# Optimization experiments

Measured on AMD Instinct MI355X. Metric: run time of the kernel, lower is better.

The kernel has to match this reference:

```python
import jax, jax.numpy as jnp
import numpy as np

IN_DIM, HID, B, T = 128, 512, 32, 2048
TAU_X, TAU = 200.0, 5


def setup_inputs() -> dict:
    key = jax.random.key(0)
    ks = jax.random.split(key, 12)
    s = 0.05
    return {
        "in_seq": jax.random.normal(ks[0], (B, T, IN_DIM), jnp.float32),
        "We1": jax.random.normal(ks[1], (IN_DIM, HID), jnp.float32) * s,
        "be1": jnp.zeros((HID,), jnp.float32),
        "We2": jax.random.normal(ks[2], (HID, HID), jnp.float32) * s,
        "be2": jnp.zeros((HID,), jnp.float32),
        "We3": jax.random.normal(ks[3], (HID, HID), jnp.float32) * s,
        "be3": jnp.zeros((HID,), jnp.float32),
        # decoder: Linear+tanh, Linear+tanh
        "Wd1": jax.random.normal(ks[4], (HID, HID), jnp.float32) * s,
        "bd1": jnp.zeros((HID,), jnp.float32),
        "Wd2": jax.random.normal(ks[5], (HID, IN_DIM), jnp.float32) * s,
        "bd2": jnp.zeros((IN_DIM,), jnp.float32),
        # recurrent weight (torch: randn * 0.1)
        "W": jax.random.normal(ks[6], (HID, HID), jnp.float32) * 0.1,
    }


def reference(in_seq, We1, be1, We2, be2, We3, be3, Wd1, bd1, Wd2, bd2, W):
    def encoder(u):
        h = jnp.tanh(u @ We1 + be1)
        h = jnp.tanh(h @ We2 + be2)
        return jnp.tanh(h @ We3 + be3)

    def decoder(h):
        h = jnp.tanh(h @ Wd1 + bd1)
        return jnp.tanh(h @ Wd2 + bd2)

    x_seq = encoder(in_seq)  # [B, T, H]
    Tlen = in_seq.shape[1]
    # teacher forcing flag per step: t % tau == 0 and t > 0
    t_idx = jnp.arange(Tlen)
    tf_flags = (t_idx % TAU == 0) & (t_idx > 0)

    xs_T = jnp.swapaxes(x_seq, 0, 1)  # [T, B, H]

    def step(x, inp):
        flag, xs_t = inp
        x = jnp.where(flag, xs_t, x)
        dx = -x + jnp.tanh(x) @ W.T
        x = x + dx / TAU_X
        return x, decoder(x)  # per-step prediction [B, in_dim]

    x0 = x_seq[:, 0, :]
    _, preds = jax.lax.scan(step, x0, (tf_flags, xs_T))  # preds: [T, B, in_dim]
    x_pred = jnp.swapaxes(preds, 0, 1)  # [B, T, in_dim]
    x_recon = decoder(x_seq)  # [B, T, in_dim]
    return (x_pred, x_recon)
```

## Files before the change

### kernel.cpp

```cpp
#include <hip/hip_runtime.h>
#include <stdint.h>

#define B_SZ  32
#define T_SZ  2048
#define IN_D  128
#define HID   512
#define NCHAIN 410
#define INV_TAUX 0.005f

typedef __attribute__((ext_vector_type(8))) short bf16x8;
typedef __attribute__((ext_vector_type(4))) float f32x4;
typedef __attribute__((ext_vector_type(4))) float float4v;
typedef __attribute__((ext_vector_type(4))) unsigned short u16x4;
typedef __attribute__((ext_vector_type(8))) unsigned short u16x8;

#define MFMA(b, a, c) __builtin_amdgcn_mfma_f32_16x16x32_bf16((b), (a), (c), 0, 0, 0)

__device__ __forceinline__ unsigned short f2bf(float x) {
  union { float f; unsigned int u; } v; v.f = x;
  unsigned int r = v.u + 0x7FFFu + ((v.u >> 16) & 1u);
  return (unsigned short)(r >> 16);
}
__device__ __forceinline__ float bf2f(unsigned short b) {
  union { unsigned int u; float f; } v; v.u = ((unsigned int)b) << 16;
  return v.f;
}
__device__ __forceinline__ float fast_tanh(float x) {
  float ax = fabsf(x);
  float e = __expf(-2.0f * ax);
  float r = (1.0f - e) * __builtin_amdgcn_rcpf(1.0f + e);
  return x < 0.0f ? -r : r;
}
__device__ __forceinline__ void gload_lds16(const void* g, void* l) {
  __builtin_amdgcn_global_load_lds(
      reinterpret_cast<__attribute__((address_space(1))) void*>(reinterpret_cast<uintptr_t>(g)),
      reinterpret_cast<__attribute__((address_space(3))) void*>(reinterpret_cast<uintptr_t>(l)),
      16, 0, 0);
}


__global__ __launch_bounds__(512) void enc5_k(
    const float* __restrict__ in_seq,
    const unsigned short* __restrict__ wt,
    const float* __restrict__ be1, const float* __restrict__ be2,
    const float* __restrict__ be3,
    const unsigned short* __restrict__ Wd1t,
    const unsigned short* __restrict__ Wd2t,
    const float* __restrict__ bd1, const float* __restrict__ bd2,
    unsigned short* __restrict__ xseq,
    float* __restrict__ outr)
{
  __shared__ __attribute__((aligned(16))) unsigned short sH[64 * 512];
  unsigned short* sA = sH;

  const int tid = threadIdx.x;
  const int m0 = blockIdx.x * 64;
  const int wave = tid >> 6, lane = tid & 63;
  const int wn = wave;
  const int lrow = lane & 15, lhi = lane >> 4, sw = lrow & 7;

#pragma unroll
  for (int p = 0; p < 2; ++p) {
    int id = (p << 9) + tid;
    int row = id >> 4, cc = id & 15;
    const float* src = in_seq + (size_t)(m0 + row) * IN_D + (cc << 3);
    float4v u0 = *(const float4v*)src;
    float4v u1 = *(const float4v*)(src + 4);
    u16x8 h;
    h[0] = f2bf(u0[0]); h[1] = f2bf(u0[1]); h[2] = f2bf(u0[2]); h[3] = f2bf(u0[3]);
    h[4] = f2bf(u1[0]); h[5] = f2bf(u1[1]); h[6] = f2bf(u1[2]); h[7] = f2bf(u1[3]);
    int slot = (cc & 8) | ((cc & 7) ^ (row & 7));
    *(u16x8*)(sA + (row << 7) + (slot << 3)) = h;
  }
  __syncthreads();

  f32x4 acc[4][4];
  const unsigned short* Bts[3] = {wt, wt + 65536, wt + 327680};
  const float* bss[3] = {be1, be2, be3};

  for (int l = 0; l < 3; ++l) {
    const int lstr = (l == 0) ? 128 : 512;
    const int nk = (l == 0) ? 4 : 16;
    const unsigned short* bl = Bts[l] + (lane << 3);
    const int nfb = (wn << 2) * nk;
    const float* bias = bss[l];

#pragma unroll
    for (int m = 0; m < 4; ++m)
#pragma unroll
      for (int n = 0; n < 4; ++n) acc[m][n] = (f32x4){0.f, 0.f, 0.f, 0.f};

    bf16x8 b0[4], b1[4];
#pragma unroll
    for (int n = 0; n < 4; ++n)
      b0[n] = *(const bf16x8*)(bl + ((nfb + n * nk) << 9));

    for (int kk = 0; kk < nk; kk += 2) {
#pragma unroll
      for (int n = 0; n < 4; ++n)
        b1[n] = *(const bf16x8*)(bl + ((nfb + n * nk + kk + 1) << 9));
      {
        const int c = (kk << 2) + lhi;
        const int slot = (c & ~7) | ((c & 7) ^ sw);
        bf16x8 af[4];
#pragma unroll
        for (int m = 0; m < 4; ++m)
          af[m] = *(const bf16x8*)(sH + (m * 16 + lrow) * lstr + (slot << 3));
#pragma unroll
        for (int n = 0; n < 4; ++n)
#pragma unroll
          for (int m = 0; m < 4; ++m)
            acc[m][n] = MFMA(b0[n], af[m], acc[m][n]);
      }
      if (kk + 2 < nk) {
#pragma unroll
        for (int n = 0; n < 4; ++n)
          b0[n] = *(const bf16x8*)(bl + ((nfb + n * nk + kk + 2) << 9));
      }
      {
        const int c = ((kk + 1) << 2) + lhi;
        const int slot = (c & ~7) | ((c & 7) ^ sw);
        bf16x8 af[4];
#pragma unroll
        for (int m = 0; m < 4; ++m)
          af[m] = *(const bf16x8*)(sH + (m * 16 + lrow) * lstr + (slot << 3));
#pragma unroll
        for (int n = 0; n < 4; ++n)
#pragma unroll
          for (int m = 0; m < 4; ++m)
            acc[m][n] = MFMA(b1[n], af[m], acc[m][n]);
      }
    }
    __syncthreads();
#pragma unroll
    for (int n = 0; n < 4; ++n) {
      const int col0 = (wn << 6) + n * 16 + (lhi << 2);
      const float4v bv = *(const float4v*)(bias + col0);
      const int c2 = col0 >> 3;
#pragma unroll
      for (int m = 0; m < 4; ++m) {
        const int row = m * 16 + lrow;
        const int slot2 = (c2 & ~7) | ((c2 & 7) ^ (row & 7));
        u16x4 h;
#pragma unroll
        for (int q = 0; q < 4; ++q) h[q] = f2bf(fast_tanh(acc[m][n][q] + bv[q]));
        *(u16x4*)(sH + (row << 9) + (slot2 << 3) + (col0 & 7)) = h;
      }
    }
    __syncthreads();
  }

#pragma unroll
  for (int p = 0; p < 8; ++p) {
    int id = (p << 9) + tid;
    int row = id >> 6, cc = id & 63;
    int slot = (cc & ~7) | ((cc & 7) ^ (row & 7));
    u16x8 v = *(const u16x8*)(sH + (row << 9) + (slot << 3));
    *(u16x8*)(xseq + ((size_t)(m0 + row) << 9) + (cc << 3)) = v;
  }

#pragma unroll
  for (int m = 0; m < 4; ++m)
#pragma unroll
    for (int n = 0; n < 4; ++n) acc[m][n] = (f32x4){0.f, 0.f, 0.f, 0.f};

  {
    const unsigned short* bl = Wd1t + (lane << 3);
    const int nfb = (wn << 2) << 4;
    bf16x8 b0[4], b1[4];
#pragma unroll
    for (int n = 0; n < 4; ++n)
      b0[n] = *(const bf16x8*)(bl + ((nfb + (n << 4)) << 9));
    for (int kk = 0; kk < 16; kk += 2) {
#pragma unroll
      for (int n = 0; n < 4; ++n)
        b1[n] = *(const bf16x8*)(bl + ((nfb + (n << 4) + kk + 1) << 9));
      {
        const int c = (kk << 2) + lhi;
        const int slot = (c & ~7) | ((c & 7) ^ sw);
        bf16x8 af[4];
#pragma unroll
        for (int m = 0; m < 4; ++m)
          af[m] = *(const bf16x8*)(sH + ((m * 16 + lrow) << 9) + (slot << 3));
#pragma unroll
        for (int n = 0; n < 4; ++n)
#pragma unroll
          for (int m = 0; m < 4; ++m)
            acc[m][n] = MFMA(b0[n], af[m], acc[m][n]);
      }
      if (kk + 2 < 16) {
#pragma unroll
        for (int n = 0; n < 4; ++n)
          b0[n] = *(const bf16x8*)(bl + ((nfb + (n << 4) + kk + 2) << 9));
      }
      {
        const int c = ((kk + 1) << 2) + lhi;
        const int slot = (c & ~7) | ((c & 7) ^ sw);
        bf16x8 af[4];
#pragma unroll
        for (int m = 0; m < 4; ++m)
          af[m] = *(const bf16x8*)(sH + ((m * 16 + lrow) << 9) + (slot << 3));
#pragma unroll
        for (int n = 0; n < 4; ++n)
#pragma unroll
          for (int m = 0; m < 4; ++m)
            acc[m][n] = MFMA(b1[n], af[m], acc[m][n]);
      }
    }
  }
  __syncthreads();
#pragma unroll
  for (int n = 0; n < 4; ++n) {
    const int col0 = (wn << 6) + n * 16 + (lhi << 2);
    const float4v bv = *(const float4v*)(bd1 + col0);
    const int c2 = col0 >> 3;
#pragma unroll
    for (int m = 0; m < 4; ++m) {
      const int row = m * 16 + lrow;
      const int slot2 = (c2 & ~7) | ((c2 & 7) ^ (row & 7));
      u16x4 h;
#pragma unroll
      for (int q = 0; q < 4; ++q) h[q] = f2bf(fast_tanh(acc[m][n][q] + bv[q]));
      *(u16x4*)(sH + (row << 9) + (slot2 << 3) + (col0 & 7)) = h;
    }
  }
  __syncthreads();

  f32x4 acc2[4];
#pragma unroll
  for (int m = 0; m < 4; ++m) acc2[m] = (f32x4){0.f, 0.f, 0.f, 0.f};

  {
    const unsigned short* bl = Wd2t + (lane << 3);
    const int nfb = wn << 4;
    bf16x8 c0, c1;
    c0 = *(const bf16x8*)(bl + ((nfb + 0) << 9));
    for (int kk = 0; kk < 16; kk += 2) {
      c1 = *(const bf16x8*)(bl + ((nfb + kk + 1) << 9));
      {
        const int c = (kk << 2) + lhi;
        const int slot = (c & ~7) | ((c & 7) ^ sw);
#pragma unroll
        for (int m = 0; m < 4; ++m) {
          bf16x8 af = *(const bf16x8*)(sH + ((m * 16 + lrow) << 9) + (slot << 3));
          acc2[m] = MFMA(c0, af, acc2[m]);
        }
      }
      if (kk + 2 < 16)
        c0 = *(const bf16x8*)(bl + ((nfb + kk + 2) << 9));
      {
        const int c = ((kk + 1) << 2) + lhi;
        const int slot = (c & ~7) | ((c & 7) ^ sw);
#pragma unroll
        for (int m = 0; m < 4; ++m) {
          bf16x8 af = *(const bf16x8*)(sH + ((m * 16 + lrow) << 9) + (slot << 3));
          acc2[m] = MFMA(c1, af, acc2[m]);
        }
      }
    }
  }
  {
    const int col0 = (wn << 4) + (lhi << 2);
    const float4v bv = *(const float4v*)(bd2 + col0);
#pragma unroll
    for (int m = 0; m < 4; ++m) {
      const int row = m * 16 + lrow;
      float4v o;
#pragma unroll
      for (int q = 0; q < 4; ++q) o[q] = fast_tanh(acc2[m][q] + bv[q]);
      *(float4v*)(outr + (size_t)(m0 + row) * IN_D + col0) = o;
    }
  }
}

__global__ __launch_bounds__(512) void dec_fused_k(
    const unsigned short* __restrict__ X,
    const unsigned short* __restrict__ Wd1t,
    const unsigned short* __restrict__ Wd2t,
    const float* __restrict__ bd1, const float* __restrict__ bd2,
    float* __restrict__ out)
{
  __shared__ __attribute__((aligned(16))) unsigned short sH[64 * 512];
  unsigned short* sX = sH;

  const int tid = threadIdx.x;
  const int m0 = blockIdx.x * 64;
  const int wave = tid >> 6, lane = tid & 63;
  const int wn = wave;
  const int lrow = lane & 15, lhi = lane >> 4, sw = lrow & 7;

  char* lX = (char*)sX + tid * 16;
#pragma unroll
  for (int p = 0; p < 8; ++p) {
    int id = (p << 9) + tid;
    int row = id >> 6, cc = id & 63;
    int gcc = (cc & ~7) | ((cc & 7) ^ (row & 7));
    gload_lds16(X + ((size_t)(m0 + row) << 9) + (gcc << 3), lX + (p << 13));
  }
  __syncthreads();

  f32x4 acc[4][4];
#pragma unroll
  for (int m = 0; m < 4; ++m)
#pragma unroll
    for (int n = 0; n < 4; ++n) acc[m][n] = (f32x4){0.f, 0.f, 0.f, 0.f};

  {
    const unsigned short* bl = Wd1t + (lane << 3);
    const int nfb = (wn << 2) << 4;
    bf16x8 b0[4], b1[4];
#pragma unroll
    for (int n = 0; n < 4; ++n)
      b0[n] = *(const bf16x8*)(bl + ((nfb + (n << 4)) << 9));
    for (int kk = 0; kk < 16; kk += 2) {
#pragma unroll
      for (int n = 0; n < 4; ++n)
        b1[n] = *(const bf16x8*)(bl + ((nfb + (n << 4) + kk + 1) << 9));
      {
        const int c = (kk << 2) + lhi;
        const int slot = (c & ~7) | ((c & 7) ^ sw);
        bf16x8 af[4];
#pragma unroll
        for (int m = 0; m < 4; ++m)
          af[m] = *(const bf16x8*)(sX + ((m * 16 + lrow) << 9) + (slot << 3));
#pragma unroll
        for (int n = 0; n < 4; ++n)
#pragma unroll
          for (int m = 0; m < 4; ++m)
            acc[m][n] = MFMA(b0[n], af[m], acc[m][n]);
      }
      if (kk + 2 < 16) {
#pragma unroll
        for (int n = 0; n < 4; ++n)
          b0[n] = *(const bf16x8*)(bl + ((nfb + (n << 4) + kk + 2) << 9));
      }
      {
        const int c = ((kk + 1) << 2) + lhi;
        const int slot = (c & ~7) | ((c & 7) ^ sw);
        bf16x8 af[4];
#pragma unroll
        for (int m = 0; m < 4; ++m)
          af[m] = *(const bf16x8*)(sX + ((m * 16 + lrow) << 9) + (slot << 3));
#pragma unroll
        for (int n = 0; n < 4; ++n)
#pragma unroll
          for (int m = 0; m < 4; ++m)
            acc[m][n] = MFMA(b1[n], af[m], acc[m][n]);
      }
    }
  }
  __syncthreads();
#pragma unroll
  for (int n = 0; n < 4; ++n) {
    const int col0 = (wn << 6) + n * 16 + (lhi << 2);
    const float4v bv = *(const float4v*)(bd1 + col0);
    const int c2 = col0 >> 3;
#pragma unroll
    for (int m = 0; m < 4; ++m) {
      const int row = m * 16 + lrow;
      const int slot2 = (c2 & ~7) | ((c2 & 7) ^ (row & 7));
      u16x4 h;
#pragma unroll
      for (int q = 0; q < 4; ++q) h[q] = f2bf(fast_tanh(acc[m][n][q] + bv[q]));
      *(u16x4*)(sH + (row << 9) + (slot2 << 3) + (col0 & 7)) = h;
    }
  }
  __syncthreads();

  f32x4 acc2[4];
#pragma unroll
  for (int m = 0; m < 4; ++m) acc2[m] = (f32x4){0.f, 0.f, 0.f, 0.f};

  {
    const unsigned short* bl = Wd2t + (lane << 3);
    const int nfb = wn << 4;
    bf16x8 c0, c1;
    c0 = *(const bf16x8*)(bl + ((nfb + 0) << 9));
    for (int kk = 0; kk < 16; kk += 2) {
      c1 = *(const bf16x8*)(bl + ((nfb + kk + 1) << 9));
      {
        const int c = (kk << 2) + lhi;
        const int slot = (c & ~7) | ((c & 7) ^ sw);
#pragma unroll
        for (int m = 0; m < 4; ++m) {
          bf16x8 af = *(const bf16x8*)(sH + ((m * 16 + lrow) << 9) + (slot << 3));
          acc2[m] = MFMA(c0, af, acc2[m]);
        }
      }
      if (kk + 2 < 16)
        c0 = *(const bf16x8*)(bl + ((nfb + kk + 2) << 9));
      {
        const int c = ((kk + 1) << 2) + lhi;
        const int slot = (c & ~7) | ((c & 7) ^ sw);
#pragma unroll
        for (int m = 0; m < 4; ++m) {
          bf16x8 af = *(const bf16x8*)(sH + ((m * 16 + lrow) << 9) + (slot << 3));
          acc2[m] = MFMA(c1, af, acc2[m]);
        }
      }
    }
  }
  {
    const int col0 = (wn << 4) + (lhi << 2);
    const float4v bv = *(const float4v*)(bd2 + col0);
#pragma unroll
    for (int m = 0; m < 4; ++m) {
      const int row = m * 16 + lrow;
      float4v o;
#pragma unroll
      for (int q = 0; q < 4; ++q) o[q] = fast_tanh(acc2[m][q] + bv[q]);
      *(float4v*)(out + (size_t)(m0 + row) * IN_D + col0) = o;
    }
  }
}

__global__ __launch_bounds__(512) void rec_all_k(
    const unsigned short* __restrict__ Wrec,
    unsigned short* __restrict__ xsall)
{
  __shared__ float xst[32][516];
  __shared__ __attribute__((aligned(16))) unsigned short sA[32 * 512];

  const int tid = threadIdx.x;
  const int chain = blockIdx.x;
  const int t0 = chain * 5;
  const int wave = tid >> 6, lane = tid & 63;
  const int wn = wave;
  const int lrow = lane & 15, lhi = lane >> 4, sw = lrow & 7;

#pragma unroll
  for (int p = 0; p < 4; ++p) {
    int id = (p << 9) + tid;
    int row = id >> 6, c8 = (id & 63) << 3;
    u16x8 v = *(const u16x8*)(xsall + (((size_t)row * T_SZ + t0) << 9) + c8);
#pragma unroll
    for (int e = 0; e < 8; ++e) xst[row][c8 + e] = bf2f(v[e]);
  }
  __syncthreads();

  const unsigned short* bl = Wrec + (lane << 3);
  const int nfb = (wn << 2) << 4;

  for (int s = 0; s < 5; ++s) {
#pragma unroll
    for (int p = 0; p < 4; ++p) {
      int id = (p << 9) + tid;
      int row = id >> 6, cc = id & 63;
      int gc = (cc & ~7) | ((cc & 7) ^ (row & 7));
      const float* src = &xst[row][gc << 3];
      float4v u0 = *(const float4v*)src;
      float4v u1 = *(const float4v*)(src + 4);
      u16x8 h;
      h[0] = f2bf(fast_tanh(u0[0])); h[1] = f2bf(fast_tanh(u0[1]));
      h[2] = f2bf(fast_tanh(u0[2])); h[3] = f2bf(fast_tanh(u0[3]));
      h[4] = f2bf(fast_tanh(u1[0])); h[5] = f2bf(fast_tanh(u1[1]));
      h[6] = f2bf(fast_tanh(u1[2])); h[7] = f2bf(fast_tanh(u1[3]));
      *(u16x8*)(sA + (row << 9) + (cc << 3)) = h;
    }
    __syncthreads();

    f32x4 acc[2][4];
#pragma unroll
    for (int m = 0; m < 2; ++m)
#pragma unroll
      for (int n = 0; n < 4; ++n) acc[m][n] = (f32x4){0.f, 0.f, 0.f, 0.f};

    bf16x8 b0[4], b1[4];
#pragma unroll
    for (int n = 0; n < 4; ++n)
      b0[n] = *(const bf16x8*)(bl + ((nfb + (n << 4)) << 9));
    for (int kk = 0; kk < 16; kk += 2) {
#pragma unroll
      for (int n = 0; n < 4; ++n)
        b1[n] = *(const bf16x8*)(bl + ((nfb + (n << 4) + kk + 1) << 9));
      {
        const int c = (kk << 2) + lhi;
        const int slot = (c & ~7) | ((c & 7) ^ sw);
        bf16x8 af0 = *(const bf16x8*)(sA + (lrow << 9) + (slot << 3));
        bf16x8 af1 = *(const bf16x8*)(sA + ((16 + lrow) << 9) + (slot << 3));
#pragma unroll
        for (int n = 0; n < 4; ++n) {
          acc[0][n] = MFMA(b0[n], af0, acc[0][n]);
          acc[1][n] = MFMA(b0[n], af1, acc[1][n]);
        }
      }
      if (kk + 2 < 16) {
#pragma unroll
        for (int n = 0; n < 4; ++n)
          b0[n] = *(const bf16x8*)(bl + ((nfb + (n << 4) + kk + 2) << 9));
      }
      {
        const int c = ((kk + 1) << 2) + lhi;
        const int slot = (c & ~7) | ((c & 7) ^ sw);
        bf16x8 af0 = *(const bf16x8*)(sA + (lrow << 9) + (slot << 3));
        bf16x8 af1 = *(const bf16x8*)(sA + ((16 + lrow) << 9) + (slot << 3));
#pragma unroll
        for (int n = 0; n < 4; ++n) {
          acc[0][n] = MFMA(b1[n], af0, acc[0][n]);
          acc[1][n] = MFMA(b1[n], af1, acc[1][n]);
        }
      }
    }
    __syncthreads();

    const int t = t0 + s;
#pragma unroll
    for (int n = 0; n < 4; ++n) {
      const int col0 = (wn << 6) + n * 16 + (lhi << 2);
#pragma unroll
      for (int m = 0; m < 2; ++m) {
        const int row = m * 16 + lrow;
        float4v x = *(const float4v*)(&xst[row][col0]);
        float4v xn;
#pragma unroll
        for (int q = 0; q < 4; ++q) xn[q] = x[q] + (acc[m][n][q] - x[q]) * INV_TAUX;
        *(float4v*)(&xst[row][col0]) = xn;
        if (t < T_SZ) {
          u16x4 h;
#pragma unroll
          for (int q = 0; q < 4; ++q) h[q] = f2bf(xn[q]);
          *(u16x4*)(xsall + ((size_t)row * T_SZ + t) * HID + col0) = h;
        }
      }
    }
    __syncthreads();
  }
}

__global__ void prep_k(const float* __restrict__ We1, const float* __restrict__ We2,
                       const float* __restrict__ We3, const float* __restrict__ Wd1,
                       const float* __restrict__ Wd2, const float* __restrict__ W,
                       unsigned short* __restrict__ wt) {
  int idx = blockIdx.x * blockDim.x + threadIdx.x;
  if (idx >= 1179648) return;
  unsigned short v;
  if (idx < 65536) {
    int i = idx, lane = (i >> 3) & 63, t2 = i >> 9;
    int kk = t2 & 3, nf = t2 >> 2;
    int n = (nf << 4) + (lane & 15), k = (kk << 5) + ((lane >> 4) << 3) + (i & 7);
    v = f2bf(We1[k * 512 + n]);
  } else if (idx < 327680) {
    int i = idx - 65536, lane = (i >> 3) & 63, t2 = i >> 9;
    int kk = t2 & 15, nf = t2 >> 4;
    int n = (nf << 4) + (lane & 15), k = (kk << 5) + ((lane >> 4) << 3) + (i & 7);
    v = f2bf(We2[k * 512 + n]);
  } else if (idx < 589824) {
    int i = idx - 327680, lane = (i >> 3) & 63, t2 = i >> 9;
    int kk = t2 & 15, nf = t2 >> 4;
    int n = (nf << 4) + (lane & 15), k = (kk << 5) + ((lane >> 4) << 3) + (i & 7);
    v = f2bf(We3[k * 512 + n]);
  } else if (idx < 851968) {
    int i = idx - 589824, lane = (i >> 3) & 63, t2 = i >> 9;
    int kk = t2 & 15, nf = t2 >> 4;
    int n = (nf << 4) + (lane & 15), k = (kk << 5) + ((lane >> 4) << 3) + (i & 7);
    v = f2bf(Wd1[k * 512 + n]);
  } else if (idx < 917504) {
    int i = idx - 851968, lane = (i >> 3) & 63, t2 = i >> 9;
    int kk = t2 & 15, nf = t2 >> 4;
    int n = (nf << 4) + (lane & 15), k = (kk << 5) + ((lane >> 4) << 3) + (i & 7);
    v = f2bf(Wd2[k * 128 + n]);
  } else {
    int i = idx - 917504, lane = (i >> 3) & 63, t2 = i >> 9;
    int kk = t2 & 15, nf = t2 >> 4;
    int n = (nf << 4) + (lane & 15), k = (kk << 5) + ((lane >> 4) << 3) + (i & 7);
    v = f2bf(W[(n << 9) + k]);
  }
  wt[idx] = v;
}

__global__ void sentinel_k(float* out, float v) { out[0] = v; }

extern "C" void kernel_launch(void* const* d_in, const int* in_sizes, int n_in,
                              void* d_out, int out_size, void* d_ws, size_t ws_size,
                              hipStream_t stream) {
  const float* in_seq = (const float*)d_in[0];
  const float* We1 = (const float*)d_in[1];
  const float* be1 = (const float*)d_in[2];
  const float* We2 = (const float*)d_in[3];
  const float* be2 = (const float*)d_in[4];
  const float* We3 = (const float*)d_in[5];
  const float* be3 = (const float*)d_in[6];
  const float* Wd1 = (const float*)d_in[7];
  const float* bd1 = (const float*)d_in[8];
  const float* Wd2 = (const float*)d_in[9];
  const float* bd2 = (const float*)d_in[10];
  const float* W   = (const float*)d_in[11];

  const int NROW = B_SZ * T_SZ;
  const size_t OFF_XSEQ = 0;
  const size_t OFF_WT   = (size_t)NROW * HID * 2;
  const size_t REQUIRED = OFF_WT + 2359296;

  float* outp = (float*)d_out;
  float* outr = outp + (size_t)NROW * IN_D;

  if (ws_size < REQUIRED) {
    sentinel_k<<<1, 1, 0, stream>>>(outp, (float)(ws_size >> 20));
    return;
  }

  char* ws = (char*)d_ws;
  unsigned short* xseq = (unsigned short*)(ws + OFF_XSEQ);
  unsigned short* wt   = (unsigned short*)(ws + OFF_WT);
  unsigned short* Wd1t = wt + 589824;
  unsigned short* Wd2t = wt + 851968;
  unsigned short* Wrec = wt + 917504;

  prep_k<<<4608, 256, 0, stream>>>(We1, We2, We3, Wd1, Wd2, W, wt);
  enc5_k<<<1024, 512, 0, stream>>>(in_seq, wt, be1, be2, be3,
                                   Wd1t, Wd2t, bd1, bd2, xseq, outr);
  rec_all_k<<<NCHAIN, 512, 0, stream>>>(Wrec, xseq);
  dec_fused_k<<<1024, 512, 0, stream>>>(xseq, Wd1t, Wd2t, bd1, bd2, outp);
}
```

Measured before the change: 439.7 us.

## Double decoder tile rows per block and stage recurrent output stores through LDS

The decoder kernel now handles 128 rows per block with 1024 threads (16 waves split 2x8), so each loaded weight fragment serves twice as many rows and the grid is halved. The recurrent kernel now writes its bf16 state into shared memory first and then stores it to global memory with 16-byte coalesced writes, replacing scattered 8-byte stores. This adds an extra barrier per recurrent step. The decoder's doubled LDS (128 KB) and 1024-thread blocks limit occupancy to one block per CU.

New measurement: 461.6 us. 1.05x slower.

```diff
diff --git a/kernel.cpp b/kernel.cpp
--- a/kernel.cpp
+++ b/kernel.cpp
@@ -273,29 +273,30 @@
   }
 }
 
-__global__ __launch_bounds__(512) void dec_fused_k(
+__global__ __launch_bounds__(1024) void dec_fused_k(
     const unsigned short* __restrict__ X,
     const unsigned short* __restrict__ Wd1t,
     const unsigned short* __restrict__ Wd2t,
     const float* __restrict__ bd1, const float* __restrict__ bd2,
     float* __restrict__ out)
 {
-  __shared__ __attribute__((aligned(16))) unsigned short sH[64 * 512];
+  __shared__ __attribute__((aligned(16))) unsigned short sH[128 * 512];
   unsigned short* sX = sH;
 
   const int tid = threadIdx.x;
-  const int m0 = blockIdx.x * 64;
+  const int m0 = blockIdx.x * 128;
   const int wave = tid >> 6, lane = tid & 63;
-  const int wn = wave;
+  const int wm = wave >> 3, wn = wave & 7;
+  const int rb = wm << 6;
   const int lrow = lane & 15, lhi = lane >> 4, sw = lrow & 7;
 
   char* lX = (char*)sX + tid * 16;
 #pragma unroll
   for (int p = 0; p < 8; ++p) {
-    int id = (p << 9) + tid;
+    int id = (p << 10) + tid;
     int row = id >> 6, cc = id & 63;
     int gcc = (cc & ~7) | ((cc & 7) ^ (row & 7));
-    gload_lds16(X + ((size_t)(m0 + row) << 9) + (gcc << 3), lX + (p << 13));
+    gload_lds16(X + ((size_t)(m0 + row) << 9) + (gcc << 3), lX + (p << 14));
   }
   __syncthreads();
 
@@ -322,7 +323,7 @@
         bf16x8 af[4];
 #pragma unroll
         for (int m = 0; m < 4; ++m)
-          af[m] = *(const bf16x8*)(sX + ((m * 16 + lrow) << 9) + (slot << 3));
+          af[m] = *(const bf16x8*)(sX + ((rb + m * 16 + lrow) << 9) + (slot << 3));
 #pragma unroll
         for (int n = 0; n < 4; ++n)
 #pragma unroll
@@ -340,7 +341,7 @@
         bf16x8 af[4];
 #pragma unroll
         for (int m = 0; m < 4; ++m)
-          af[m] = *(const bf16x8*)(sX + ((m * 16 + lrow) << 9) + (slot << 3));
+          af[m] = *(const bf16x8*)(sX + ((rb + m * 16 + lrow) << 9) + (slot << 3));
 #pragma unroll
         for (int n = 0; n < 4; ++n)
 #pragma unroll
@@ -357,7 +358,7 @@
     const int c2 = col0 >> 3;
 #pragma unroll
     for (int m = 0; m < 4; ++m) {
-      const int row = m * 16 + lrow;
+      const int row = rb + m * 16 + lrow;
       const int slot2 = (c2 & ~7) | ((c2 & 7) ^ (row & 7));
       u16x4 h;
 #pragma unroll
@@ -383,7 +384,7 @@
         const int slot = (c & ~7) | ((c & 7) ^ sw);
 #pragma unroll
         for (int m = 0; m < 4; ++m) {
-          bf16x8 af = *(const bf16x8*)(sH + ((m * 16 + lrow) << 9) + (slot << 3));
+          bf16x8 af = *(const bf16x8*)(sH + ((rb + m * 16 + lrow) << 9) + (slot << 3));
           acc2[m] = MFMA(c0, af, acc2[m]);
         }
       }
@@ -394,7 +395,7 @@
         const int slot = (c & ~7) | ((c & 7) ^ sw);
 #pragma unroll
         for (int m = 0; m < 4; ++m) {
-          bf16x8 af = *(const bf16x8*)(sH + ((m * 16 + lrow) << 9) + (slot << 3));
+          bf16x8 af = *(const bf16x8*)(sH + ((rb + m * 16 + lrow) << 9) + (slot << 3));
           acc2[m] = MFMA(c1, af, acc2[m]);
         }
       }
@@ -405,7 +406,7 @@
     const float4v bv = *(const float4v*)(bd2 + col0);
 #pragma unroll
     for (int m = 0; m < 4; ++m) {
-      const int row = m * 16 + lrow;
+      const int row = rb + m * 16 + lrow;
       float4v o;
 #pragma unroll
       for (int q = 0; q < 4; ++q) o[q] = fast_tanh(acc2[m][q] + bv[q]);
@@ -503,7 +504,6 @@
     }
     __syncthreads();
 
-    const int t = t0 + s;
 #pragma unroll
     for (int n = 0; n < 4; ++n) {
       const int col0 = (wn << 6) + n * 16 + (lhi << 2);
@@ -512,15 +512,26 @@
         const int row = m * 16 + lrow;
         float4v x = *(const float4v*)(&xst[row][col0]);
         float4v xn;
-#pragma unroll
-        for (int q = 0; q < 4; ++q) xn[q] = x[q] + (acc[m][n][q] - x[q]) * INV_TAUX;
+        u16x4 h;
+#pragma unroll
+        for (int q = 0; q < 4; ++q) {
+          xn[q] = x[q] + (acc[m][n][q] - x[q]) * INV_TAUX;
+          h[q] = f2bf(xn[q]);
+        }
         *(float4v*)(&xst[row][col0]) = xn;
-        if (t < T_SZ) {
-          u16x4 h;
-#pragma unroll
-          for (int q = 0; q < 4; ++q) h[q] = f2bf(xn[q]);
-          *(u16x4*)(xsall + ((size_t)row * T_SZ + t) * HID + col0) = h;
-        }
+        *(u16x4*)(sA + (row << 9) + col0) = h;
+      }
+    }
+    __syncthreads();
+
+    const int t = t0 + s;
+    if (t < T_SZ) {
+#pragma unroll
+      for (int p = 0; p < 4; ++p) {
+        int id = (p << 9) + tid;
+        int row = id >> 6, c8 = (id & 63) << 3;
+        u16x8 v = *(const u16x8*)(sA + (row << 9) + c8);
+        *(u16x8*)(xsall + (((size_t)row * T_SZ + t) << 9) + c8) = v;
       }
     }
     __syncthreads();
@@ -610,5 +621,5 @@
   enc5_k<<<1024, 512, 0, stream>>>(in_seq, wt, be1, be2, be3,
                                    Wd1t, Wd2t, bd1, bd2, xseq, outr);
   rec_all_k<<<NCHAIN, 512, 0, stream>>>(Wrec, xseq);
-  dec_fused_k<<<1024, 512, 0, stream>>>(xseq, Wd1t, Wd2t, bd1, bd2, outp);
-}
+  dec_fused_k<<<512, 1024, 0, stream>>>(xseq, Wd1t, Wd2t, bd1, bd2, outp);
+}
```
